# Performance work log

Measured on AMD Instinct MI355X. Metric: run time of the kernel, lower is better.

Reference implementation:

```python
import math
import jax, jax.numpy as jnp
import numpy as np

NUM_HEADS = 16
EPS = 1e-5


def _layernorm(x, g, b):
    mu = jnp.mean(x, axis=-1, keepdims=True)
    var = jnp.mean(jnp.square(x - mu), axis=-1, keepdims=True)
    return (x - mu) * jax.lax.rsqrt(var + EPS) * g + b


def setup_inputs() -> dict:
    key = jax.random.key(0)
    ks = jax.random.split(key, 8)
    B, S, D, F = 2, 2048, 1024, 4096
    s = 1.0 / math.sqrt(D)
    return {
        "x": jax.random.normal(ks[0], (B, S, D), jnp.float32),
        "wq": jax.random.normal(ks[1], (D, D), jnp.float32) * s,
        "wk": jax.random.normal(ks[2], (D, D), jnp.float32) * s,
        "wv": jax.random.normal(ks[3], (D, D), jnp.float32) * s,
        "wo": jax.random.normal(ks[4], (D, D), jnp.float32) * s,
        "w1": jax.random.normal(ks[5], (D, F), jnp.float32) * s,
        "b1": jnp.zeros((F,), jnp.float32),
        "w2": jax.random.normal(ks[6], (F, D), jnp.float32) / math.sqrt(F),
        "b2": jnp.zeros((D,), jnp.float32),
        "ln1_g": jnp.ones((D,), jnp.float32),
        "ln1_b": jnp.zeros((D,), jnp.float32),
        "ln2_g": jnp.ones((D,), jnp.float32),
        "ln2_b": jnp.zeros((D,), jnp.float32),
        "theta": jax.random.normal(ks[7], (1,), jnp.float32),
    }


def reference(x, wq, wk, wv, wo, w1, b1, w2, b2, ln1_g, ln1_b, ln2_g, ln2_b, theta):
    B, S, D = x.shape
    H = NUM_HEADS
    dk = D // H

    # QKV projections (no bias), split heads -> [B, H, S, dk]
    def split(t):
        return t.reshape(B, S, H, dk).transpose(0, 2, 1, 3)

    q = split(x @ wq)
    k = split(x @ wk)
    v = split(x @ wv)

    scores = jnp.einsum("bhqd,bhkd->bhqk", q, k) / math.sqrt(dk)
    attn = jax.nn.softmax(scores, axis=-1)
    ctx = jnp.einsum("bhqk,bhkd->bhqd", attn, v)
    ctx = ctx.transpose(0, 2, 1, 3).reshape(B, S, D)
    attn_out = ctx @ wo

    # Quantum gate: RX(theta) then <PauliZ> = cos(theta); sigmoid -> scalar gate
    gate = jax.nn.sigmoid(jnp.cos(theta[0]))
    attn_out = attn_out * gate

    x1 = _layernorm(x + attn_out, ln1_g, ln1_b)
    ffn = jax.nn.relu(x1 @ w1 + b1) @ w2 + b2
    return _layernorm(x1 + ffn, ln2_g, ln2_b)
```

## Files before the change

### kernel.cpp

```cpp
#include <hip/hip_runtime.h>
#include <cstdint>
#include <cstddef>

#define SEQ 2048
#define DMODEL 1024
#define FDIM 4096
#define NH 16
#define DK 64
#define MROWS 4096

typedef __attribute__((ext_vector_type(8))) short short8;
typedef __attribute__((ext_vector_type(4))) short s16x4;
typedef __attribute__((ext_vector_type(4))) float f32x4;

__device__ __forceinline__ short f2bf(float f) {
    unsigned u = __float_as_uint(f);
    u += 0x7FFFu + ((u >> 16) & 1u);
    return (short)(u >> 16);
}

__device__ __forceinline__ void gload_lds16(const void* g, void* l) {
    __builtin_amdgcn_global_load_lds(
        (const __attribute__((address_space(1))) void*)g,
        (__attribute__((address_space(3))) void*)l,
        16, 0, 0);
}

__global__ __launch_bounds__(256) void cast_kernel(const float* __restrict__ in,
                                                   short* __restrict__ out, int n4) {
    int i = blockIdx.x * 256 + threadIdx.x;
    if (i < n4) {
        float4 v = ((const float4*)in)[i];
        s16x4 ob = { f2bf(v.x), f2bf(v.y), f2bf(v.z), f2bf(v.w) };
        *(s16x4*)(out + (size_t)i * 4) = ob;
    }
}

__global__ void transpose_cast(const float* __restrict__ in, short* __restrict__ out,
                               int R, int C) {
    __shared__ float tile[32][33];
    const int c0 = blockIdx.x * 32, r0 = blockIdx.y * 32;
    const int tx = threadIdx.x, ty = threadIdx.y;
#pragma unroll
    for (int jj = 0; jj < 4; jj++) {
        int j = jj * 8 + ty;
        tile[j][tx] = in[(size_t)(r0 + j) * C + c0 + tx];
    }
    __syncthreads();
#pragma unroll
    for (int jj = 0; jj < 4; jj++) {
        int j = jj * 8 + ty;
        out[(size_t)(c0 + j) * R + r0 + tx] = f2bf(tile[tx][j]);
    }
}

#define MODE_QKV 0
#define MODE_O   1
#define MODE_H   2
#define MODE_F   3

template<int BN>
__global__ __launch_bounds__(256) void gemm_bt(
    const short* __restrict__ A, const short* __restrict__ Bt,
    const int M, const int N, const int K, const int mode,
    const float* __restrict__ p0, const float* __restrict__ p1,
    void* __restrict__ outp)
{
    __shared__ __align__(16) short ldsA[128 * 32];
    __shared__ __align__(16) short ldsB[BN * 32];
    const int t = threadIdx.x;
    const int nbx = N / BN;
    const int q8 = gridDim.x >> 3;
    const int swz = (blockIdx.x & 7) * q8 + (blockIdx.x >> 3);
    const int bx = swz % nbx;
    const int by = swz / nbx;
    const int brow = by << 7, bcol = bx * BN;
    const int l = t & 63, w = t >> 6;
    const int lr = l & 15, lk = l >> 4;
    const int sr = t >> 2, sc8 = (t & 3) << 3;

    constexpr int RF = (BN == 128) ? 4 : 2;
    const int wrow = (BN == 128) ? ((w >> 1) * 64) : (w * 32);
    const int wcol = (BN == 128) ? ((w & 1) * 64) : 0;

    f32x4 acc[RF][4] = {};

    const short* gA = A + (size_t)(brow + sr) * K + sc8;
    const short* gB = Bt + (size_t)(bcol + sr) * K + sc8;

    for (int k0 = 0; k0 < K; k0 += 32) {
        gload_lds16(gA + k0,                     &ldsA[t * 8]);
        gload_lds16(gA + (size_t)64 * K + k0,    &ldsA[2048 + t * 8]);
        gload_lds16(gB + k0,                     &ldsB[t * 8]);
        if (BN == 128)
            gload_lds16(gB + (size_t)64 * K + k0, &ldsB[2048 + t * 8]);
        __syncthreads();
        short8 af[RF], bfr[4];
#pragma unroll
        for (int i = 0; i < RF; i++)
            af[i] = *(const short8*)&ldsA[(wrow + i * 16 + lr) * 32 + lk * 8];
#pragma unroll
        for (int j = 0; j < 4; j++)
            bfr[j] = *(const short8*)&ldsB[(wcol + j * 16 + lr) * 32 + lk * 8];
#pragma unroll
        for (int i = 0; i < RF; i++)
#pragma unroll
            for (int j = 0; j < 4; j++)
                acc[i][j] = __builtin_amdgcn_mfma_f32_16x16x32_bf16(af[i], bfr[j], acc[i][j], 0, 0, 0);
        __syncthreads();
    }

    float gate = 0.f;
    if (mode == MODE_O) gate = 1.f / (1.f + expf(-cosf(p1[0])));

#pragma unroll
    for (int i = 0; i < RF; i++) {
        const int mrow0 = brow + wrow + i * 16 + lk * 4;
#pragma unroll
        for (int j = 0; j < 4; j++) {
            const int gcol = bcol + wcol + j * 16 + lr;
#pragma unroll
            for (int r = 0; r < 4; r++) {
                const int m = mrow0 + r;
                float v = acc[i][j][r];
                if (mode == MODE_QKV) {
                    int which = gcol >> 10;
                    int nn = gcol & 1023;
                    int h = nn >> 6, d = nn & 63;
                    int b = m >> 11, s = m & 2047;
                    if (which == 0) v *= 0.125f;
                    size_t idx = (which == 2)
                        ? ((((size_t)(b * NH + h)) * DK + d) * SEQ + s)
                        : ((((size_t)(b * NH + h)) * SEQ + s) * DK + d);
                    ((short*)outp)[(size_t)which * ((size_t)MROWS * DMODEL) + idx] = f2bf(v);
                } else if (mode == MODE_O) {
                    size_t idx = (size_t)m * N + gcol;
                    ((float*)outp)[idx] = p0[idx] + gate * v;
                } else if (mode == MODE_H) {
                    float hv = v + p0[gcol];
                    ((short*)outp)[(size_t)m * N + gcol] = f2bf(hv > 0.f ? hv : 0.f);
                } else {
                    size_t idx = (size_t)m * N + gcol;
                    ((float*)outp)[idx] = v + p0[gcol] + p1[idx];
                }
            }
        }
    }
}

__global__ __launch_bounds__(256) void attn_kernel(
    const short* __restrict__ q, const short* __restrict__ k,
    const short* __restrict__ vt, short* __restrict__ ctx)
{
    __shared__ __align__(16) short ldsK[64 * 64];
    __shared__ __align__(16) short ldsV[64 * 64];
    __shared__ __align__(16) short ldsP[64 * 64];
    const int t = threadIdx.x;
    const int w = t >> 6, l = t & 63, lr = l & 15, lk = l >> 4;
    const int bh = blockIdx.x >> 5;
    const int qt = blockIdx.x & 31;
    const int b = bh >> 4, h = bh & 15;
    const size_t koff = (size_t)bh * SEQ * DK;
    const size_t voff = (size_t)bh * DK * SEQ;

    const int qrow = qt * 64 + w * 16 + lr;
    short8 aq[2];
    aq[0] = *(const short8*)&q[koff + (size_t)qrow * DK + lk * 8];
    aq[1] = *(const short8*)&q[koff + (size_t)qrow * DK + 32 + lk * 8];

    f32x4 o[4] = {};
    float mrow[4] = {-1e30f, -1e30f, -1e30f, -1e30f};
    float den[4] = {0.f, 0.f, 0.f, 0.f};

    const int strow = t >> 3;
    const int c8 = (t & 7) ^ (strow & 7);
    const short* gK0 = k + koff + (size_t)strow * DK + c8 * 8;
    const short* gV0 = vt + voff + (size_t)strow * SEQ + c8 * 8;

    for (int s0 = 0; s0 < SEQ; s0 += 64) {
        gload_lds16(gK0 + (size_t)s0 * DK,        &ldsK[t * 8]);
        gload_lds16(gK0 + (size_t)(s0 + 32) * DK, &ldsK[2048 + t * 8]);
        gload_lds16(gV0 + s0,                     &ldsV[t * 8]);
        gload_lds16(gV0 + s0 + (size_t)32 * SEQ,  &ldsV[2048 + t * 8]);
        __syncthreads();

        f32x4 sc[4] = {};
#pragma unroll
        for (int kk = 0; kk < 2; kk++) {
#pragma unroll
            for (int nt = 0; nt < 4; nt++) {
                const int row = nt * 16 + lr;
                short8 bk = *(const short8*)&ldsK[row * 64 + (((kk * 4 + lk) ^ (row & 7)) * 8)];
                sc[nt] = __builtin_amdgcn_mfma_f32_16x16x32_bf16(aq[kk], bk, sc[nt], 0, 0, 0);
            }
        }

#pragma unroll
        for (int r = 0; r < 4; r++) {
            float pm = fmaxf(fmaxf(sc[0][r], sc[1][r]), fmaxf(sc[2][r], sc[3][r]));
            pm = fmaxf(pm, __shfl_xor(pm, 1));
            pm = fmaxf(pm, __shfl_xor(pm, 2));
            pm = fmaxf(pm, __shfl_xor(pm, 4));
            pm = fmaxf(pm, __shfl_xor(pm, 8));
            float mnew = fmaxf(mrow[r], pm);
            float scale = __expf(mrow[r] - mnew);
            float ps = 0.f;
#pragma unroll
            for (int nt = 0; nt < 4; nt++) {
                float p = __expf(sc[nt][r] - mnew);
                sc[nt][r] = p;
                ps += p;
            }
            ps += __shfl_xor(ps, 1);
            ps += __shfl_xor(ps, 2);
            ps += __shfl_xor(ps, 4);
            ps += __shfl_xor(ps, 8);
            den[r] = den[r] * scale + ps;
            mrow[r] = mnew;
#pragma unroll
            for (int nt = 0; nt < 4; nt++) o[nt][r] *= scale;
        }

#pragma unroll
        for (int r = 0; r < 4; r++) {
            const int prow = w * 16 + lk * 4 + r;
#pragma unroll
            for (int nt = 0; nt < 4; nt++) {
                const int col16 = nt * 2 + (lr >> 3);
                const int sw = col16 ^ (prow & 7);
                ldsP[prow * 64 + sw * 8 + (lr & 7)] = f2bf(sc[nt][r]);
            }
        }

#pragma unroll
        for (int kk = 0; kk < 2; kk++) {
            const int prow2 = w * 16 + lr;
            short8 pa = *(const short8*)&ldsP[prow2 * 64 + (((kk * 4 + lk) ^ (prow2 & 7)) * 8)];
#pragma unroll
            for (int nt = 0; nt < 4; nt++) {
                const int vrow = nt * 16 + lr;
                short8 bv = *(const short8*)&ldsV[vrow * 64 + (((kk * 4 + lk) ^ (vrow & 7)) * 8)];
                o[nt] = __builtin_amdgcn_mfma_f32_16x16x32_bf16(pa, bv, o[nt], 0, 0, 0);
            }
        }
        __syncthreads();
    }

#pragma unroll
    for (int r = 0; r < 4; r++) {
        const float inv = 1.f / den[r];
        const int s = qt * 64 + w * 16 + lk * 4 + r;
        const size_t base = ((size_t)b * SEQ + s) * DMODEL + h * DK;
#pragma unroll
        for (int nt = 0; nt < 4; nt++)
            ctx[base + nt * 16 + lr] = f2bf(o[nt][r] * inv);
    }
}

__global__ __launch_bounds__(256) void ln_kernel(
    const float* __restrict__ y, const float* __restrict__ g,
    const float* __restrict__ bb, short* __restrict__ out_bf,
    float* __restrict__ out_f)
{
    const int row = blockIdx.x;
    const int t = threadIdx.x;
    const float4 v = ((const float4*)(y + (size_t)row * DMODEL))[t];
    float s = v.x + v.y + v.z + v.w;
    float ss = v.x * v.x + v.y * v.y + v.z * v.z + v.w * v.w;
#pragma unroll
    for (int off = 32; off > 0; off >>= 1) {
        s  += __shfl_down(s, off);
        ss += __shfl_down(ss, off);
    }
    __shared__ float red[8];
    const int w = t >> 6, l = t & 63;
    if (l == 0) { red[w] = s; red[4 + w] = ss; }
    __syncthreads();
    s  = red[0] + red[1] + red[2] + red[3];
    ss = red[4] + red[5] + red[6] + red[7];
    const float mu = s * (1.f / DMODEL);
    const float var = ss * (1.f / DMODEL) - mu * mu;
    const float rstd = rsqrtf(var + 1e-5f);
    const float4 gg = ((const float4*)g)[t];
    const float4 bv = ((const float4*)bb)[t];
    float o0 = (v.x - mu) * rstd * gg.x + bv.x;
    float o1 = (v.y - mu) * rstd * gg.y + bv.y;
    float o2 = (v.z - mu) * rstd * gg.z + bv.z;
    float o3 = (v.w - mu) * rstd * gg.w + bv.w;
    if (out_f) ((float4*)(out_f + (size_t)row * DMODEL))[t] = make_float4(o0, o1, o2, o3);
    if (out_bf) {
        s16x4 ob = { f2bf(o0), f2bf(o1), f2bf(o2), f2bf(o3) };
        *(s16x4*)(out_bf + (size_t)row * DMODEL + t * 4) = ob;
    }
}

extern "C" void kernel_launch(void* const* d_in, const int* in_sizes, int n_in,
                              void* d_out, int out_size, void* d_ws, size_t ws_size,
                              hipStream_t stream)
{
    const float* x     = (const float*)d_in[0];
    const float* wq    = (const float*)d_in[1];
    const float* wk    = (const float*)d_in[2];
    const float* wv    = (const float*)d_in[3];
    const float* wo    = (const float*)d_in[4];
    const float* w1    = (const float*)d_in[5];
    const float* b1    = (const float*)d_in[6];
    const float* w2    = (const float*)d_in[7];
    const float* b2    = (const float*)d_in[8];
    const float* ln1_g = (const float*)d_in[9];
    const float* ln1_b = (const float*)d_in[10];
    const float* ln2_g = (const float*)d_in[11];
    const float* ln2_b = (const float*)d_in[12];
    const float* theta = (const float*)d_in[13];

    short* wsS   = (short*)d_ws;
    short* xb    = wsS;
    short* wqkvT = wsS + 4194304;
    short* woT   = wsS + 7340032;
    short* w1T   = wsS + 8388608;
    short* w2T   = wsS + 12582912;
    short* qb    = wsS + 16777216;
    short* ctxb  = wsS + 29360128;
    short* x1b   = wsS + 33554432;
    short* hb    = qb;
    float* fbase = (float*)((char*)d_ws + 75497472);
    float* y1    = fbase;
    float* x1f   = fbase + 4194304;
    if (ws_size < 109051904) return;

    dim3 t32(32, 8, 1);
    cast_kernel<<<4096, 256, 0, stream>>>(x, xb, 1048576);
    transpose_cast<<<dim3(32, 32), t32, 0, stream>>>(wq, wqkvT,           DMODEL, DMODEL);
    transpose_cast<<<dim3(32, 32), t32, 0, stream>>>(wk, wqkvT + 1048576, DMODEL, DMODEL);
    transpose_cast<<<dim3(32, 32), t32, 0, stream>>>(wv, wqkvT + 2097152, DMODEL, DMODEL);
    transpose_cast<<<dim3(32, 32), t32, 0, stream>>>(wo, woT,             DMODEL, DMODEL);
    transpose_cast<<<dim3(128, 32), t32, 0, stream>>>(w1, w1T, DMODEL, FDIM);
    transpose_cast<<<dim3(32, 128), t32, 0, stream>>>(w2, w2T, FDIM, DMODEL);

    gemm_bt<128><<<768, 256, 0, stream>>>(xb, wqkvT, MROWS, 3072, DMODEL, MODE_QKV,
                                          nullptr, nullptr, qb);
    attn_kernel<<<1024, 256, 0, stream>>>(qb, qb + 4194304, qb + 8388608, ctxb);
    gemm_bt<64><<<512, 256, 0, stream>>>(ctxb, woT, MROWS, DMODEL, DMODEL, MODE_O,
                                         x, theta, y1);
    ln_kernel<<<4096, 256, 0, stream>>>(y1, ln1_g, ln1_b, x1b, x1f);
    gemm_bt<128><<<1024, 256, 0, stream>>>(x1b, w1T, MROWS, FDIM, DMODEL, MODE_H,
                                           b1, nullptr, hb);
    gemm_bt<64><<<512, 256, 0, stream>>>(hb, w2T, MROWS, DMODEL, FDIM, MODE_F,
                                         b2, x1f, y1);
    ln_kernel<<<4096, 256, 0, stream>>>(y1, ln2_g, ln2_b, nullptr, (float*)d_out);
}
```

Measured before the change: 487.9 us.

## Double-buffer K/V tiles and transpose QK^T in attention kernel, with lazy rescale

The attention kernel now double-buffers K and V tiles in LDS, prefetching the next 64-key tile while computing on the current one, so global loads overlap with compute. The QK^T MFMA operands are swapped so each lane holds one query row's scores. This turns the row-max and row-sum reductions from four cross-lane shuffles per row into two, and lets P be written to per-wave LDS as packed bf16 pairs. The online softmax also skips rescaling the accumulator when the new max stays within 8 of the running max, which saves exp and multiply work at the cost of a small overflow-headroom tradeoff.

```diff
diff --git a/kernel.cpp b/kernel.cpp
--- a/kernel.cpp
+++ b/kernel.cpp
@@ -152,9 +152,9 @@
     const short* __restrict__ q, const short* __restrict__ k,
     const short* __restrict__ vt, short* __restrict__ ctx)
 {
-    __shared__ __align__(16) short ldsK[64 * 64];
-    __shared__ __align__(16) short ldsV[64 * 64];
-    __shared__ __align__(16) short ldsP[64 * 64];
+    __shared__ __align__(16) short ldsK[2 * 64 * 64];
+    __shared__ __align__(16) short ldsV[2 * 64 * 64];
+    __shared__ __align__(16) unsigned int ldsP[4 * 512];
     const int t = threadIdx.x;
     const int w = t >> 6, l = t & 63, lr = l & 15, lk = l >> 4;
     const int bh = blockIdx.x >> 5;
@@ -169,20 +169,32 @@
     aq[1] = *(const short8*)&q[koff + (size_t)qrow * DK + 32 + lk * 8];
 
     f32x4 o[4] = {};
-    float mrow[4] = {-1e30f, -1e30f, -1e30f, -1e30f};
-    float den[4] = {0.f, 0.f, 0.f, 0.f};
+    float mrow = -1e30f, den = 0.f;
 
     const int strow = t >> 3;
     const int c8 = (t & 7) ^ (strow & 7);
     const short* gK0 = k + koff + (size_t)strow * DK + c8 * 8;
     const short* gV0 = vt + voff + (size_t)strow * SEQ + c8 * 8;
 
-    for (int s0 = 0; s0 < SEQ; s0 += 64) {
-        gload_lds16(gK0 + (size_t)s0 * DK,        &ldsK[t * 8]);
-        gload_lds16(gK0 + (size_t)(s0 + 32) * DK, &ldsK[2048 + t * 8]);
-        gload_lds16(gV0 + s0,                     &ldsV[t * 8]);
-        gload_lds16(gV0 + s0 + (size_t)32 * SEQ,  &ldsV[2048 + t * 8]);
-        __syncthreads();
+    gload_lds16(gK0,                    &ldsK[t * 8]);
+    gload_lds16(gK0 + (size_t)32 * DK,  &ldsK[2048 + t * 8]);
+    gload_lds16(gV0,                    &ldsV[t * 8]);
+    gload_lds16(gV0 + (size_t)32 * SEQ, &ldsV[2048 + t * 8]);
+    __syncthreads();
+
+    unsigned int* Pw = &ldsP[w * 512 + lr * 32];
+    int cur = 0;
+    for (int it = 0; it < SEQ / 64; ++it) {
+        const int s0n = (it + 1) * 64;
+        if (s0n < SEQ) {
+            const int nb = cur ^ 1;
+            gload_lds16(gK0 + (size_t)s0n * DK,        &ldsK[nb * 4096 + t * 8]);
+            gload_lds16(gK0 + (size_t)(s0n + 32) * DK, &ldsK[nb * 4096 + 2048 + t * 8]);
+            gload_lds16(gV0 + s0n,                     &ldsV[nb * 4096 + t * 8]);
+            gload_lds16(gV0 + s0n + (size_t)32 * SEQ,  &ldsV[nb * 4096 + 2048 + t * 8]);
+        }
+        const short* bK = &ldsK[cur * 4096];
+        const short* bV = &ldsV[cur * 4096];
 
         f32x4 sc[4] = {};
 #pragma unroll
@@ -190,70 +202,75 @@
 #pragma unroll
             for (int nt = 0; nt < 4; nt++) {
                 const int row = nt * 16 + lr;
-                short8 bk = *(const short8*)&ldsK[row * 64 + (((kk * 4 + lk) ^ (row & 7)) * 8)];
-                sc[nt] = __builtin_amdgcn_mfma_f32_16x16x32_bf16(aq[kk], bk, sc[nt], 0, 0, 0);
+                short8 kf = *(const short8*)&bK[row * 64 + (((kk * 4 + lk) ^ (row & 7)) * 8)];
+                sc[nt] = __builtin_amdgcn_mfma_f32_16x16x32_bf16(kf, aq[kk], sc[nt], 0, 0, 0);
             }
         }
 
-#pragma unroll
-        for (int r = 0; r < 4; r++) {
-            float pm = fmaxf(fmaxf(sc[0][r], sc[1][r]), fmaxf(sc[2][r], sc[3][r]));
-            pm = fmaxf(pm, __shfl_xor(pm, 1));
-            pm = fmaxf(pm, __shfl_xor(pm, 2));
-            pm = fmaxf(pm, __shfl_xor(pm, 4));
-            pm = fmaxf(pm, __shfl_xor(pm, 8));
-            float mnew = fmaxf(mrow[r], pm);
-            float scale = __expf(mrow[r] - mnew);
-            float ps = 0.f;
-#pragma unroll
-            for (int nt = 0; nt < 4; nt++) {
-                float p = __expf(sc[nt][r] - mnew);
-                sc[nt][r] = p;
-                ps += p;
+        float pm = fmaxf(fmaxf(fmaxf(sc[0][0], sc[0][1]), fmaxf(sc[0][2], sc[0][3])),
+                   fmaxf(fmaxf(fmaxf(sc[1][0], sc[1][1]), fmaxf(sc[1][2], sc[1][3])),
+                   fmaxf(fmaxf(fmaxf(sc[2][0], sc[2][1]), fmaxf(sc[2][2], sc[2][3])),
+                         fmaxf(fmaxf(sc[3][0], sc[3][1]), fmaxf(sc[3][2], sc[3][3])))));
+        pm = fmaxf(pm, __shfl_xor(pm, 16));
+        pm = fmaxf(pm, __shfl_xor(pm, 32));
+        const bool defer = __all(pm <= mrow + 8.0f);
+        const float mnew = defer ? mrow : fmaxf(mrow, pm);
+
+        float ps = 0.f;
+#pragma unroll
+        for (int nt = 0; nt < 4; nt++) {
+            float p0 = __expf(sc[nt][0] - mnew);
+            float p1 = __expf(sc[nt][1] - mnew);
+            float p2 = __expf(sc[nt][2] - mnew);
+            float p3 = __expf(sc[nt][3] - mnew);
+            ps += (p0 + p1) + (p2 + p3);
+            unsigned int d0 = (unsigned int)(unsigned short)f2bf(p0)
+                            | ((unsigned int)(unsigned short)f2bf(p1) << 16);
+            unsigned int d1 = (unsigned int)(unsigned short)f2bf(p2)
+                            | ((unsigned int)(unsigned short)f2bf(p3) << 16);
+            const int cidx = (((nt * 2 + (lk >> 1)) ^ (lr & 7)) << 2) + ((lk & 1) << 1);
+            Pw[cidx]     = d0;
+            Pw[cidx + 1] = d1;
+        }
+        ps += __shfl_xor(ps, 16);
+        ps += __shfl_xor(ps, 32);
+        if (defer) {
+            den += ps;
+        } else {
+            const float scale = __expf(mrow - mnew);
+            den = den * scale + ps;
+            mrow = mnew;
+#pragma unroll
+            for (int r = 0; r < 4; r++) {
+                const float sf = __shfl(scale, (lk << 2) + r);
+#pragma unroll
+                for (int nt2 = 0; nt2 < 4; nt2++) o[nt2][r] *= sf;
             }
-            ps += __shfl_xor(ps, 1);
-            ps += __shfl_xor(ps, 2);
-            ps += __shfl_xor(ps, 4);
-            ps += __shfl_xor(ps, 8);
-            den[r] = den[r] * scale + ps;
-            mrow[r] = mnew;
-#pragma unroll
-            for (int nt = 0; nt < 4; nt++) o[nt][r] *= scale;
-        }
-
-#pragma unroll
-        for (int r = 0; r < 4; r++) {
-            const int prow = w * 16 + lk * 4 + r;
-#pragma unroll
-            for (int nt = 0; nt < 4; nt++) {
-                const int col16 = nt * 2 + (lr >> 3);
-                const int sw = col16 ^ (prow & 7);
-                ldsP[prow * 64 + sw * 8 + (lr & 7)] = f2bf(sc[nt][r]);
+        }
+
+#pragma unroll
+        for (int kk = 0; kk < 2; kk++) {
+            short8 pa = *(const short8*)&Pw[((kk * 4 + lk) ^ (lr & 7)) << 2];
+#pragma unroll
+            for (int nt2 = 0; nt2 < 4; nt2++) {
+                const int vrow = nt2 * 16 + lr;
+                short8 bv = *(const short8*)&bV[vrow * 64 + (((kk * 4 + lk) ^ (vrow & 7)) * 8)];
+                o[nt2] = __builtin_amdgcn_mfma_f32_16x16x32_bf16(pa, bv, o[nt2], 0, 0, 0);
             }
         }
-
-#pragma unroll
-        for (int kk = 0; kk < 2; kk++) {
-            const int prow2 = w * 16 + lr;
-            short8 pa = *(const short8*)&ldsP[prow2 * 64 + (((kk * 4 + lk) ^ (prow2 & 7)) * 8)];
-#pragma unroll
-            for (int nt = 0; nt < 4; nt++) {
-                const int vrow = nt * 16 + lr;
-                short8 bv = *(const short8*)&ldsV[vrow * 64 + (((kk * 4 + lk) ^ (vrow & 7)) * 8)];
-                o[nt] = __builtin_amdgcn_mfma_f32_16x16x32_bf16(pa, bv, o[nt], 0, 0, 0);
-            }
-        }
         __syncthreads();
+        cur ^= 1;
     }
 
 #pragma unroll
     for (int r = 0; r < 4; r++) {
-        const float inv = 1.f / den[r];
-        const int s = qt * 64 + w * 16 + lk * 4 + r;
+        const float dn = __shfl(den, (lk << 2) + r);
+        const float inv = 1.f / dn;
+        const int s = qt * 64 + w * 16 + (lk << 2) + r;
         const size_t base = ((size_t)b * SEQ + s) * DMODEL + h * DK;
 #pragma unroll
-        for (int nt = 0; nt < 4; nt++)
-            ctx[base + nt * 16 + lr] = f2bf(o[nt][r] * inv);
+        for (int nt2 = 0; nt2 < 4; nt2++)
+            ctx[base + nt2 * 16 + lr] = f2bf(o[nt2][r] * inv);
     }
 }
 
```

After: 447.6 us. 8.3% less time.
